# Optimization experiments

Hardware: AMD Instinct MI355X
Metric: run time of the kernel (lower is better)

The kernel has to match this reference:

```python
import jax, jax.numpy as jnp
import numpy as np

LATENT = 16
CTRL = 8
BLN = 128
MU = 0.1
EPS = 0.01
DT = 1.0
HID = 64


def _mlp(x, W1, b1, W2, b2, W3, b3):
    # two-hidden-layer tanh MLP (matches nn.Sequential(Linear,Tanh,Linear,Tanh,Linear))
    h = jnp.tanh(x @ W1.T + b1)
    h = jnp.tanh(h @ W2.T + b2)
    return h @ W3.T + b3


def setup_inputs() -> dict:
    key = jax.random.key(0)
    ks = jax.random.split(key, 16)
    B = 131072

    def w(k, shape):
        fan_in = shape[-1]
        return (jax.random.normal(k, shape, dtype=jnp.float32) / np.sqrt(fan_in)).astype(jnp.float32)

    inp = {
        "z": jax.random.normal(ks[0], (B, LATENT), dtype=jnp.float32),
        "u": jax.random.normal(ks[1], (B, CTRL), dtype=jnp.float32),
        # PLNet/BiLipNet Hamiltonian surrogate params: H(z)=0.5||mu*z + W_h2 tanh(W_h1 z + b_h1)||^2
        "Wh1": w(ks[2], (BLN, LATENT)),
        "bh1": jnp.zeros((BLN,), dtype=jnp.float32),
        "Wh2": w(ks[3], (LATENT, BLN)) * 0.5,
        # JR_net: latent -> 64 -> 64 -> 2*latent^2
        "W1_jr": w(ks[4], (HID, LATENT)),
        "b1_jr": jnp.zeros((HID,), dtype=jnp.float32),
        "W2_jr": w(ks[5], (HID, HID)),
        "b2_jr": jnp.zeros((HID,), dtype=jnp.float32),
        "W3_jr": w(ks[6], (2 * LATENT * LATENT, HID)) * 0.1,
        "b3_jr": jnp.zeros((2 * LATENT * LATENT,), dtype=jnp.float32),
        # Bnet: latent -> 64 -> 64 -> latent*control
        "W1_b": w(ks[7], (HID, LATENT)),
        "b1_b": jnp.zeros((HID,), dtype=jnp.float32),
        "W2_b": w(ks[8], (HID, HID)),
        "b2_b": jnp.zeros((HID,), dtype=jnp.float32),
        "W3_b": w(ks[9], (LATENT * CTRL, HID)) * 0.1,
        "b3_b": jnp.zeros((LATENT * CTRL,), dtype=jnp.float32),
    }
    return inp


def _compute_dz_and_output(z, u, Wh1, bh1, Wh2,
                           W1_jr, b1_jr, W2_jr, b2_jr, W3_jr, b3_jr,
                           W1_b, b1_b, W2_b, b2_b, W3_b, b3_b):
    B = z.shape[0]
    d = LATENT

    # H(z) = 0.5 ||f(z)||^2, f = mu*z + Wh2 tanh(Wh1 z + bh1)  (PLNet over BiLipNet surrogate)
    def H_sum(zz):
        f = MU * zz + jnp.tanh(zz @ Wh1.T + bh1) @ Wh2.T
        return 0.5 * jnp.sum(f * f)

    gH = jax.grad(H_sum)(z)                                  # [B, d]

    JR_out = _mlp(z, W1_jr, b1_jr, W2_jr, b2_jr, W3_jr, b3_jr)  # [B, 2d^2]
    Jm = JR_out[:, : d * d].reshape(B, d, d)
    Rf = JR_out[:, d * d:].reshape(B, d, d)
    J = Jm - jnp.swapaxes(Jm, 1, 2)                          # skew-symmetric
    R = jnp.einsum("bik,bjk->bij", Rf, Rf)                    # PSD

    Bmat = _mlp(z, W1_b, b1_b, W2_b, b2_b, W3_b, b3_b).reshape(B, d, CTRL)
    Bu = jnp.einsum("bdm,bm->bd", Bmat, u)

    dz = jnp.einsum("bij,bj->bi", J - R, gH) + Bu - EPS * gH
    y_pred = jnp.einsum("bdm,bd->bm", Bmat, gH)
    return dz, y_pred


def reference(z, u, Wh1, bh1, Wh2,
              W1_jr, b1_jr, W2_jr, b2_jr, W3_jr, b3_jr,
              W1_b, b1_b, W2_b, b2_b, W3_b, b3_b):
    args = (Wh1, bh1, Wh2, W1_jr, b1_jr, W2_jr, b2_jr, W3_jr, b3_jr,
            W1_b, b1_b, W2_b, b2_b, W3_b, b3_b)
    dz1, _ = _compute_dz_and_output(z, u, *args)
    z1 = z + DT * dz1
    dz2, y_pred = _compute_dz_and_output(z1, u, *args)
    z_next = z + 0.5 * DT * (dz1 + dz2)
    return (z_next, y_pred)
```

## Files before the change

### kernel.cpp

```cpp
#include <hip/hip_runtime.h>

#define THREADS 256
#define MU_C  0.1f
#define EPS_C 0.01f

typedef short bf16x8 __attribute__((ext_vector_type(8)));
typedef bf16x8 bf16x8_a __attribute__((may_alias));
typedef float f32x4 __attribute__((ext_vector_type(4)));
typedef f32x4 f32x4_a __attribute__((may_alias));
typedef float f32_a __attribute__((may_alias));
typedef unsigned uint2v __attribute__((ext_vector_type(2)));
typedef uint2v uint2_a __attribute__((may_alias));
typedef unsigned u32_a __attribute__((may_alias));
typedef unsigned short u16_a __attribute__((may_alias));

#define MFMA(a, b, c) __builtin_amdgcn_mfma_f32_16x16x32_bf16((a), (b), (c), 0, 0, 0)

#define T_WH1   0
#define T_WH2   8
#define T_WH2T  12
#define T_WH1T  20
#define T_W1JR  24
#define T_W2JR  28
#define T_JMN   36
#define T_JMT   68
#define T_RFN   100
#define T_RFT   132
#define T_W1B   164
#define T_W2B   168
#define T_BMN   176
#define T_BMT   192
#define T_JBN   208
#define T_JBT   209
#define T_RBN   210
#define T_RBT   211
#define T_BBN   212
#define NTILES  213

__device__ __forceinline__ float ftanh(float x) {
    float e = __builtin_amdgcn_exp2f(x * 2.88539008177792681472f);
    return 1.0f - 2.0f * __builtin_amdgcn_rcpf(e + 1.0f);
}
__device__ __forceinline__ short bfrn(float f) {
    unsigned u = __float_as_uint(f);
    return (short)((u + 0x8000u) >> 16);
}
__device__ __forceinline__ float bf2f(unsigned lo16) {
    return __uint_as_float(lo16 << 16);
}
__device__ __forceinline__ unsigned pk2(float lo, float hi) {
    return ((unsigned)(unsigned short)bfrn(hi) << 16) | (unsigned short)bfrn(lo);
}
__device__ __forceinline__ bf16x8 wsB(const short* __restrict__ ws, int tile, int lane) {
    return *reinterpret_cast<const bf16x8*>(ws + (size_t)((tile << 6) + lane) * 8);
}
__device__ __forceinline__ bf16x8 ldsA(const short* base, int strideS, int lane, int k0) {
    return *reinterpret_cast<const bf16x8_a*>(base + (lane & 15) * strideS + k0 + (lane >> 4) * 8);
}

__global__ __launch_bounds__(256)
void pack_weights(const float* __restrict__ Wh1, const float* __restrict__ bh1,
                  const float* __restrict__ Wh2,
                  const float* __restrict__ W1jr, const float* __restrict__ b1jr,
                  const float* __restrict__ W2jr, const float* __restrict__ W3jr,
                  const float* __restrict__ b3jr,
                  const float* __restrict__ W1b, const float* __restrict__ b1b,
                  const float* __restrict__ W2b, const float* __restrict__ W3b,
                  const float* __restrict__ b3b,
                  short* __restrict__ ws)
{
    const int id = blockIdx.x * 256 + threadIdx.x;
    if (id >= NTILES * 64) return;
    const int tile = id >> 6, lane = id & 63;
    const int j2 = lane & 15, g = lane >> 4;
    bf16x8 f;
#pragma unroll
    for (int jj = 0; jj < 8; ++jj) {
        const int k = g * 8 + jj;
        float x = 0.f;
        if (tile < T_WH2) {
            int n0 = (tile - T_WH1) * 16;
            if (g < 2) x = Wh1[(n0 + j2) * 16 + k];
            else if (k == 16) x = bh1[n0 + j2];
        } else if (tile < T_WH2T) {
            int kt = tile - T_WH2;
            x = Wh2[j2 * 128 + kt * 32 + k];
        } else if (tile < T_WH1T) {
            if (g < 2) x = Wh2[k * 128 + (tile - T_WH2T) * 16 + j2];
        } else if (tile < T_W1JR) {
            int kt = tile - T_WH1T;
            x = Wh1[(kt * 32 + k) * 16 + j2];
        } else if (tile < T_W2JR) {
            int n0 = (tile - T_W1JR) * 16;
            if (g < 2) x = W1jr[(n0 + j2) * 16 + k];
            else if (k == 16) x = b1jr[n0 + j2];
        } else if (tile < T_JMN) {
            int q = tile - T_W2JR; int nt = q >> 1, kt = q & 1;
            x = W2jr[(nt * 16 + j2) * 64 + kt * 32 + k];
        } else if (tile < T_JMT) {
            int q = tile - T_JMN; int n = q >> 1, kt = q & 1;
            x = W3jr[(n * 16 + j2) * 64 + kt * 32 + k];
        } else if (tile < T_RFN) {
            int q = tile - T_JMT; int t = q >> 1, kt = q & 1;
            x = W3jr[(j2 * 16 + t) * 64 + kt * 32 + k];
        } else if (tile < T_RFT) {
            int q = tile - T_RFN; int n = q >> 1, kt = q & 1;
            x = W3jr[(256 + n * 16 + j2) * 64 + kt * 32 + k];
        } else if (tile < T_W1B) {
            int q = tile - T_RFT; int t = q >> 1, kt = q & 1;
            x = W3jr[(256 + j2 * 16 + t) * 64 + kt * 32 + k];
        } else if (tile < T_W2B) {
            int n0 = (tile - T_W1B) * 16;
            if (g < 2) x = W1b[(n0 + j2) * 16 + k];
            else if (k == 16) x = b1b[n0 + j2];
        } else if (tile < T_BMN) {
            int q = tile - T_W2B; int nt = q >> 1, kt = q & 1;
            x = W2b[(nt * 16 + j2) * 64 + kt * 32 + k];
        } else if (tile < T_BMT) {
            int q = tile - T_BMN; int n = q >> 1, kt = q & 1;
            x = W3b[(n * 16 + j2) * 64 + kt * 32 + k];
        } else if (tile < T_JBN) {
            int q = tile - T_BMT; int m = q >> 1, kt = q & 1;
            x = W3b[(j2 * 8 + m) * 64 + kt * 32 + k];
        } else if (tile == T_JBN) {
            if (k < 16) x = b3jr[k * 16 + j2];
        } else if (tile == T_JBT) {
            if (k < 16) x = b3jr[j2 * 16 + k];
        } else if (tile == T_RBN) {
            if (k < 16) x = b3jr[256 + k * 16 + j2];
        } else if (tile == T_RBT) {
            if (k < 16) x = b3jr[256 + j2 * 16 + k];
        } else {
            if (k < 16 && j2 < 8) x = b3b[k * 8 + j2];
        }
        f[jj] = bfrn(x);
    }
    reinterpret_cast<bf16x8*>(ws)[id] = f;
}

struct __align__(16) WaveLds {
    short zt [16 * 40];
    short fvt[16 * 40];
    char  act[4608];
    float gHf[16 * 20];
    float uf [16 * 9];
};
struct __align__(16) BlockLds {
    WaveLds w[4];
    float bias[256];
};

__global__ __launch_bounds__(THREADS)
__attribute__((amdgpu_waves_per_eu(2, 4)))
void ph_mfma_kernel(const float* __restrict__ zg, const float* __restrict__ ug,
                    const float* __restrict__ b2jr, const float* __restrict__ b2b,
                    const float* __restrict__ b3b,
                    const short* __restrict__ ws,
                    float* __restrict__ out, int B)
{
    __shared__ BlockLds L;
    const int tid  = threadIdx.x;
    const int lane = tid & 63;
    const int wid  = tid >> 6;
    const int j2   = lane & 15;
    const int g    = lane >> 4;
    const int g4   = g * 4;
    const int rowbase = blockIdx.x * 64 + wid * 16;
    if (blockIdx.x * 64 >= B) return;

    WaveLds& Wv = L.w[wid];
    short* t1s = (short*)Wv.act;
    short* h1t = (short*)Wv.act;
    short* h2t = (short*)(Wv.act + 2304);
    short* rft = (short*)Wv.act;

    if (tid < 256) {
        float v;
        if      (tid < 64)  v = b2jr[tid];
        else if (tid < 128) v = b2b[tid - 64];
        else                v = b3b[tid - 128];
        L.bias[tid] = v;
    }
    if (lane < 16) {
        u32_a* p = (u32_a*)&Wv.zt[lane * 40 + 16];
        p[0] = 0x00003F80u;
#pragma unroll
        for (int i = 1; i < 8; ++i) p[i] = 0u;
        u32_a* q = (u32_a*)&Wv.fvt[lane * 40 + 16];
#pragma unroll
        for (int i = 0; i < 8; ++i) q[i] = 0u;
    }
    for (int i = lane; i < 128; i += 64) {
        int r = i >> 3, m = i & 7;
        Wv.uf[r * 9 + m] = ug[(size_t)(rowbase + r) * 8 + m];
    }
    float zReg[4];
    {
        float4 zv = *reinterpret_cast<const float4*>(zg + (size_t)(rowbase + j2) * 16 + g4);
        zReg[0] = zv.x; zReg[1] = zv.y; zReg[2] = zv.z; zReg[3] = zv.w;
        *(uint2_a*)&Wv.zt[j2 * 40 + g4] = (uint2v){pk2(zv.x, zv.y), pk2(zv.z, zv.w)};
    }
    __syncthreads();

#pragma unroll 1
    for (int pass = 0; pass < 2; ++pass) {
        bf16x8 bZ = ldsA(Wv.zt, 40, lane, 0);
        float dzAcc[4], fvReg[4];

#pragma unroll 4
        for (int nt = 0; nt < 8; ++nt) {
            f32x4 acc = {0.f, 0.f, 0.f, 0.f};
            acc = MFMA(wsB(ws, T_WH1 + nt, lane), bZ, acc);
            unsigned p0 = pk2(ftanh(acc[0]), ftanh(acc[1]));
            unsigned p1 = pk2(ftanh(acc[2]), ftanh(acc[3]));
            *(uint2_a*)&t1s[j2 * 136 + nt * 16 + g4] = (uint2v){p0, p1};
        }
        {
            f32x4 acc = {0.f, 0.f, 0.f, 0.f};
#pragma unroll 2
            for (int kt = 0; kt < 4; ++kt)
                acc = MFMA(wsB(ws, T_WH2 + kt, lane), ldsA(t1s, 136, lane, kt * 32), acc);
#pragma unroll
            for (int r = 0; r < 4; ++r) fvReg[r] = acc[r] + MU_C * zReg[r];
            *(uint2_a*)&Wv.fvt[j2 * 40 + g4] = (uint2v){pk2(fvReg[0], fvReg[1]), pk2(fvReg[2], fvReg[3])};
        }
        {
            bf16x8 bF = ldsA(Wv.fvt, 40, lane, 0);
#pragma unroll 4
            for (int nt = 0; nt < 8; ++nt) {
                f32x4 acc = {0.f, 0.f, 0.f, 0.f};
                acc = MFMA(wsB(ws, T_WH2T + nt, lane), bF, acc);
                uint2v tp = *(const uint2_a*)&t1s[j2 * 136 + nt * 16 + g4];
                float t0 = bf2f(tp[0] & 0xffffu), t1v = bf2f(tp[0] >> 16);
                float t2 = bf2f(tp[1] & 0xffffu), t3 = bf2f(tp[1] >> 16);
                unsigned p0 = pk2((1.f - t0 * t0) * acc[0], (1.f - t1v * t1v) * acc[1]);
                unsigned p1 = pk2((1.f - t2 * t2) * acc[2], (1.f - t3 * t3) * acc[3]);
                *(uint2_a*)&t1s[j2 * 136 + nt * 16 + g4] = (uint2v){p0, p1};
            }
        }
        {
            f32x4 acc = {0.f, 0.f, 0.f, 0.f};
#pragma unroll 2
            for (int kt = 0; kt < 4; ++kt)
                acc = MFMA(wsB(ws, T_WH1T + kt, lane), ldsA(t1s, 136, lane, kt * 32), acc);
            float gh0 = acc[0] + MU_C * fvReg[0], gh1 = acc[1] + MU_C * fvReg[1];
            float gh2 = acc[2] + MU_C * fvReg[2], gh3 = acc[3] + MU_C * fvReg[3];
            *(f32x4_a*)&Wv.gHf[j2 * 20 + g4] = (f32x4){gh0, gh1, gh2, gh3};
            *(uint2_a*)&Wv.fvt[j2 * 40 + g4] = (uint2v){pk2(gh0, gh1), pk2(gh2, gh3)};
            dzAcc[0] = -EPS_C * gh0; dzAcc[1] = -EPS_C * gh1;
            dzAcc[2] = -EPS_C * gh2; dzAcc[3] = -EPS_C * gh3;
        }
#pragma unroll 2
        for (int nt = 0; nt < 4; ++nt) {
            f32x4 acc = {0.f, 0.f, 0.f, 0.f};
            acc = MFMA(wsB(ws, T_W1JR + nt, lane), bZ, acc);
            *(uint2_a*)&h1t[j2 * 72 + nt * 16 + g4] =
                (uint2v){pk2(ftanh(acc[0]), ftanh(acc[1])), pk2(ftanh(acc[2]), ftanh(acc[3]))};
        }
        {
            bf16x8 b0 = ldsA(h1t, 72, lane, 0);
            bf16x8 b1 = ldsA(h1t, 72, lane, 32);
#pragma unroll 2
            for (int nt = 0; nt < 4; ++nt) {
                f32x4 acc = {0.f, 0.f, 0.f, 0.f};
                acc = MFMA(wsB(ws, T_W2JR + nt * 2 + 0, lane), b0, acc);
                acc = MFMA(wsB(ws, T_W2JR + nt * 2 + 1, lane), b1, acc);
                *(uint2_a*)&h2t[j2 * 72 + nt * 16 + g4] =
                    (uint2v){pk2(ftanh(acc[0] + L.bias[nt * 16 + g4 + 0]),
                                 ftanh(acc[1] + L.bias[nt * 16 + g4 + 1])),
                             pk2(ftanh(acc[2] + L.bias[nt * 16 + g4 + 2]),
                                 ftanh(acc[3] + L.bias[nt * 16 + g4 + 3]))};
            }
        }
        {
            bf16x8 bH0 = ldsA(h2t, 72, lane, 0);
            bf16x8 bH1 = ldsA(h2t, 72, lane, 32);
            bf16x8 bG  = ldsA(Wv.fvt, 40, lane, 0);
            {
                f32x4 bn = {0.f, 0.f, 0.f, 0.f};
                bn = MFMA(wsB(ws, T_JBN, lane), bG, bn);
                f32x4 bt = {0.f, 0.f, 0.f, 0.f};
                bt = MFMA(wsB(ws, T_JBT, lane), bG, bt);
#pragma unroll
                for (int r = 0; r < 4; ++r) dzAcc[r] += bt[r] - bn[r];
            }
#pragma unroll 4
            for (int n = 0; n < 16; ++n) {
                f32x4 acc = {0.f, 0.f, 0.f, 0.f};
                acc = MFMA(wsB(ws, T_JMN + 2 * n + 0, lane), bH0, acc);
                acc = MFMA(wsB(ws, T_JMN + 2 * n + 1, lane), bH1, acc);
                float gh = *(const f32_a*)&Wv.gHf[j2 * 20 + n];
#pragma unroll
                for (int r = 0; r < 4; ++r) dzAcc[r] -= acc[r] * gh;
            }
#pragma unroll 4
            for (int t = 0; t < 16; ++t) {
                f32x4 acc = {0.f, 0.f, 0.f, 0.f};
                acc = MFMA(wsB(ws, T_JMT + 2 * t + 0, lane), bH0, acc);
                acc = MFMA(wsB(ws, T_JMT + 2 * t + 1, lane), bH1, acc);
                float gh = *(const f32_a*)&Wv.gHf[j2 * 20 + t];
#pragma unroll
                for (int r = 0; r < 4; ++r) dzAcc[r] += acc[r] * gh;
            }
            {
                float rAcc[4] = {0.f, 0.f, 0.f, 0.f};
#pragma unroll 4
                for (int n = 0; n < 16; ++n) {
                    f32x4 acc = {0.f, 0.f, 0.f, 0.f};
                    acc = MFMA(wsB(ws, T_RFN + 2 * n + 0, lane), bH0, acc);
                    acc = MFMA(wsB(ws, T_RFN + 2 * n + 1, lane), bH1, acc);
                    float gh = *(const f32_a*)&Wv.gHf[j2 * 20 + n];
#pragma unroll
                    for (int r = 0; r < 4; ++r) rAcc[r] += acc[r] * gh;
                }
                f32x4 rb = {0.f, 0.f, 0.f, 0.f};
                rb = MFMA(wsB(ws, T_RBN, lane), bG, rb);
#pragma unroll
                for (int r = 0; r < 4; ++r) rAcc[r] += rb[r];
                *(uint2_a*)&rft[j2 * 40 + g4] = (uint2v){pk2(rAcc[0], rAcc[1]), pk2(rAcc[2], rAcc[3])};
                if (lane < 16) {
                    u32_a* p = (u32_a*)&rft[lane * 40 + 16];
#pragma unroll
                    for (int i = 0; i < 8; ++i) p[i] = 0u;
                }
            }
            {
                f32x4 rtb = {0.f, 0.f, 0.f, 0.f};
                rtb = MFMA(wsB(ws, T_RBT, lane), ldsA(rft, 40, lane, 0), rtb);
#pragma unroll
                for (int r = 0; r < 4; ++r) dzAcc[r] -= rtb[r];
            }
#pragma unroll 4
            for (int t = 0; t < 16; ++t) {
                f32x4 acc = {0.f, 0.f, 0.f, 0.f};
                acc = MFMA(wsB(ws, T_RFT + 2 * t + 0, lane), bH0, acc);
                acc = MFMA(wsB(ws, T_RFT + 2 * t + 1, lane), bH1, acc);
                float rv = bf2f(*(const u16_a*)&rft[j2 * 40 + t]);
#pragma unroll
                for (int r = 0; r < 4; ++r) dzAcc[r] -= acc[r] * rv;
            }
        }
#pragma unroll 2
        for (int nt = 0; nt < 4; ++nt) {
            f32x4 acc = {0.f, 0.f, 0.f, 0.f};
            acc = MFMA(wsB(ws, T_W1B + nt, lane), bZ, acc);
            *(uint2_a*)&h1t[j2 * 72 + nt * 16 + g4] =
                (uint2v){pk2(ftanh(acc[0]), ftanh(acc[1])), pk2(ftanh(acc[2]), ftanh(acc[3]))};
        }
        {
            bf16x8 b0 = ldsA(h1t, 72, lane, 0);
            bf16x8 b1 = ldsA(h1t, 72, lane, 32);
#pragma unroll 2
            for (int nt = 0; nt < 4; ++nt) {
                f32x4 acc = {0.f, 0.f, 0.f, 0.f};
                acc = MFMA(wsB(ws, T_W2B + nt * 2 + 0, lane), b0, acc);
                acc = MFMA(wsB(ws, T_W2B + nt * 2 + 1, lane), b1, acc);
                *(uint2_a*)&h2t[j2 * 72 + nt * 16 + g4] =
                    (uint2v){pk2(ftanh(acc[0] + L.bias[64 + nt * 16 + g4 + 0]),
                                 ftanh(acc[1] + L.bias[64 + nt * 16 + g4 + 1])),
                             pk2(ftanh(acc[2] + L.bias[64 + nt * 16 + g4 + 2]),
                                 ftanh(acc[3] + L.bias[64 + nt * 16 + g4 + 3]))};
            }
        }
        float yAcc[4] = {0.f, 0.f, 0.f, 0.f};
        f32x4 yb = {0.f, 0.f, 0.f, 0.f};
        {
            bf16x8 b0 = ldsA(h2t, 72, lane, 0);
            bf16x8 b1 = ldsA(h2t, 72, lane, 32);
            bf16x8 bG = ldsA(Wv.fvt, 40, lane, 0);
            yb = MFMA(wsB(ws, T_BBN, lane), bG, yb);
#pragma unroll 4
            for (int n = 0; n < 8; ++n) {
                f32x4 acc = {0.f, 0.f, 0.f, 0.f};
                acc = MFMA(wsB(ws, T_BMN + 2 * n + 0, lane), b0, acc);
                acc = MFMA(wsB(ws, T_BMN + 2 * n + 1, lane), b1, acc);
                float gh = *(const f32_a*)&Wv.gHf[j2 * 20 + 2 * n + (g >> 1)];
#pragma unroll
                for (int r = 0; r < 4; ++r) yAcc[r] += acc[r] * gh;
            }
#pragma unroll 4
            for (int m = 0; m < 8; ++m) {
                f32x4 acc = {0.f, 0.f, 0.f, 0.f};
                acc = MFMA(wsB(ws, T_BMT + 2 * m + 0, lane), b0, acc);
                acc = MFMA(wsB(ws, T_BMT + 2 * m + 1, lane), b1, acc);
                float um = *(const f32_a*)&Wv.uf[j2 * 9 + m];
#pragma unroll
                for (int r = 0; r < 4; ++r)
                    dzAcc[r] += (acc[r] + L.bias[128 + (g4 + r) * 8 + m]) * um;
            }
        }
        float* op = out + (size_t)(rowbase + j2) * 16 + g4;
        if (pass == 0) {
            float4 o;
            o.x = zReg[0] + 0.5f * dzAcc[0]; o.y = zReg[1] + 0.5f * dzAcc[1];
            o.z = zReg[2] + 0.5f * dzAcc[2]; o.w = zReg[3] + 0.5f * dzAcc[3];
            *reinterpret_cast<float4*>(op) = o;
#pragma unroll
            for (int r = 0; r < 4; ++r) zReg[r] += dzAcc[r];
            *(uint2_a*)&Wv.zt[j2 * 40 + g4] = (uint2v){pk2(zReg[0], zReg[1]), pk2(zReg[2], zReg[3])};
        } else {
            float4 o = *reinterpret_cast<const float4*>(op);
            o.x += 0.5f * dzAcc[0]; o.y += 0.5f * dzAcc[1];
            o.z += 0.5f * dzAcc[2]; o.w += 0.5f * dzAcc[3];
            *reinterpret_cast<float4*>(op) = o;
            float yv0 = yAcc[0] + __shfl_xor(yAcc[0], 32) + yb[0];
            float yv1 = yAcc[1] + __shfl_xor(yAcc[1], 32) + yb[1];
            float yv2 = yAcc[2] + __shfl_xor(yAcc[2], 32) + yb[2];
            float yv3 = yAcc[3] + __shfl_xor(yAcc[3], 32) + yb[3];
            if (g < 2) {
                float4 ys; ys.x = yv0; ys.y = yv1; ys.z = yv2; ys.w = yv3;
                *reinterpret_cast<float4*>(out + (size_t)B * 16 + (size_t)(rowbase + j2) * 8 + g4) = ys;
            }
        }
    }
}

extern "C" void kernel_launch(void* const* d_in, const int* in_sizes, int n_in,
                              void* d_out, int out_size, void* d_ws, size_t ws_size,
                              hipStream_t stream) {
    const float* zg   = (const float*)d_in[0];
    const float* ug   = (const float*)d_in[1];
    const float* Wh1  = (const float*)d_in[2];
    const float* bh1  = (const float*)d_in[3];
    const float* Wh2  = (const float*)d_in[4];
    const float* W1jr = (const float*)d_in[5];
    const float* b1jr = (const float*)d_in[6];
    const float* W2jr = (const float*)d_in[7];
    const float* b2jr = (const float*)d_in[8];
    const float* W3jr = (const float*)d_in[9];
    const float* b3jr = (const float*)d_in[10];
    const float* W1b  = (const float*)d_in[11];
    const float* b1b  = (const float*)d_in[12];
    const float* W2b  = (const float*)d_in[13];
    const float* b2b  = (const float*)d_in[14];
    const float* W3b  = (const float*)d_in[15];
    const float* b3b  = (const float*)d_in[16];

    short* ws = (short*)d_ws;
    const int B = in_sizes[0] / 16;

    hipLaunchKernelGGL(pack_weights, dim3((NTILES * 64 + 255) / 256), dim3(256), 0, stream,
                       Wh1, bh1, Wh2, W1jr, b1jr, W2jr, W3jr, b3jr,
                       W1b, b1b, W2b, W3b, b3b, ws);

    const int grid = (B + 63) / 64;
    hipLaunchKernelGGL(ph_mfma_kernel, dim3(grid), dim3(THREADS), 0, stream,
                       zg, ug, b2jr, b2b, b3b, ws, (float*)d_out, B);
}
```

Baseline: 115.3 us.

## Process two 16-row tiles per wave to reuse weight fragments across MFMAs

Each wave now handles 32 rows as two independent 16-row tiles. Every weight fragment loaded from global memory feeds two MFMAs instead of one, and the two independent accumulator chains add instruction-level parallelism. Per-wave LDS buffers are duplicated and the grid is halved. The cost is doubled LDS and higher register pressure per block, which may lower occupancy. The bias term of y is now folded into the accumulator before the cross-lane reduction.

```diff
diff --git a/kernel.cpp b/kernel.cpp
--- a/kernel.cpp
+++ b/kernel.cpp
@@ -14,7 +14,10 @@
 typedef unsigned u32_a __attribute__((may_alias));
 typedef unsigned short u16_a __attribute__((may_alias));
 
-#define MFMA(a, b, c) __builtin_amdgcn_mfma_f32_16x16x32_bf16((a), (b), (c), 0, 0, 0)
+__device__ __forceinline__ f32x4 MFMA(bf16x8 a, bf16x8 b, f32x4 c) {
+    return __builtin_amdgcn_mfma_f32_16x16x32_bf16(a, b, c, 0, 0, 0);
+}
+__device__ __forceinline__ f32x4 Z4() { f32x4 z = {0.f, 0.f, 0.f, 0.f}; return z; }
 
 #define T_WH1   0
 #define T_WH2   8
@@ -139,11 +142,11 @@
 }
 
 struct __align__(16) WaveLds {
-    short zt [16 * 40];
-    short fvt[16 * 40];
-    char  act[4608];
-    float gHf[16 * 20];
-    float uf [16 * 9];
+    short zt [2][16 * 40];
+    short fvt[2][16 * 40];
+    char  act[2][4608];
+    float gHf[2][16 * 20];
+    float uf [2][16 * 9];
 };
 struct __align__(16) BlockLds {
     WaveLds w[4];
@@ -165,14 +168,14 @@
     const int j2   = lane & 15;
     const int g    = lane >> 4;
     const int g4   = g * 4;
-    const int rowbase = blockIdx.x * 64 + wid * 16;
-    if (blockIdx.x * 64 >= B) return;
+    const int rowbase = blockIdx.x * 128 + wid * 32;
+    if (blockIdx.x * 128 >= B) return;
 
     WaveLds& Wv = L.w[wid];
-    short* t1s = (short*)Wv.act;
-    short* h1t = (short*)Wv.act;
-    short* h2t = (short*)(Wv.act + 2304);
-    short* rft = (short*)Wv.act;
+    short* t1p[2] = {(short*)Wv.act[0], (short*)Wv.act[1]};
+    short* h1p[2] = {(short*)Wv.act[0], (short*)Wv.act[1]};
+    short* h2p[2] = {(short*)(Wv.act[0] + 2304), (short*)(Wv.act[1] + 2304)};
+    short* rfp[2] = {(short*)Wv.act[0], (short*)Wv.act[1]};
 
     if (tid < 256) {
         float v;
@@ -182,234 +185,340 @@
         L.bias[tid] = v;
     }
     if (lane < 16) {
-        u32_a* p = (u32_a*)&Wv.zt[lane * 40 + 16];
-        p[0] = 0x00003F80u;
-#pragma unroll
-        for (int i = 1; i < 8; ++i) p[i] = 0u;
-        u32_a* q = (u32_a*)&Wv.fvt[lane * 40 + 16];
-#pragma unroll
-        for (int i = 0; i < 8; ++i) q[i] = 0u;
+#pragma unroll
+        for (int rt = 0; rt < 2; ++rt) {
+            u32_a* p = (u32_a*)&Wv.zt[rt][lane * 40 + 16];
+            p[0] = 0x00003F80u;
+#pragma unroll
+            for (int i = 1; i < 8; ++i) p[i] = 0u;
+            u32_a* q = (u32_a*)&Wv.fvt[rt][lane * 40 + 16];
+#pragma unroll
+            for (int i = 0; i < 8; ++i) q[i] = 0u;
+        }
     }
-    for (int i = lane; i < 128; i += 64) {
-        int r = i >> 3, m = i & 7;
-        Wv.uf[r * 9 + m] = ug[(size_t)(rowbase + r) * 8 + m];
+    for (int i = lane; i < 256; i += 64) {
+        int rt = i >> 7, r = (i >> 3) & 15, m = i & 7;
+        Wv.uf[rt][r * 9 + m] = ug[(size_t)(rowbase + rt * 16 + r) * 8 + m];
     }
-    float zReg[4];
-    {
-        float4 zv = *reinterpret_cast<const float4*>(zg + (size_t)(rowbase + j2) * 16 + g4);
-        zReg[0] = zv.x; zReg[1] = zv.y; zReg[2] = zv.z; zReg[3] = zv.w;
-        *(uint2_a*)&Wv.zt[j2 * 40 + g4] = (uint2v){pk2(zv.x, zv.y), pk2(zv.z, zv.w)};
+    float zReg[2][4];
+#pragma unroll
+    for (int rt = 0; rt < 2; ++rt) {
+        float4 zv = *reinterpret_cast<const float4*>(zg + (size_t)(rowbase + rt * 16 + j2) * 16 + g4);
+        zReg[rt][0] = zv.x; zReg[rt][1] = zv.y; zReg[rt][2] = zv.z; zReg[rt][3] = zv.w;
+        *(uint2_a*)&Wv.zt[rt][j2 * 40 + g4] = (uint2v){pk2(zv.x, zv.y), pk2(zv.z, zv.w)};
     }
     __syncthreads();
 
 #pragma unroll 1
     for (int pass = 0; pass < 2; ++pass) {
-        bf16x8 bZ = ldsA(Wv.zt, 40, lane, 0);
-        float dzAcc[4], fvReg[4];
-
-#pragma unroll 4
+        bf16x8 bZ0 = ldsA(Wv.zt[0], 40, lane, 0);
+        bf16x8 bZ1 = ldsA(Wv.zt[1], 40, lane, 0);
+        float dzAcc[2][4], fvReg[2][4];
+
+#pragma unroll 2
         for (int nt = 0; nt < 8; ++nt) {
-            f32x4 acc = {0.f, 0.f, 0.f, 0.f};
-            acc = MFMA(wsB(ws, T_WH1 + nt, lane), bZ, acc);
-            unsigned p0 = pk2(ftanh(acc[0]), ftanh(acc[1]));
-            unsigned p1 = pk2(ftanh(acc[2]), ftanh(acc[3]));
-            *(uint2_a*)&t1s[j2 * 136 + nt * 16 + g4] = (uint2v){p0, p1};
-        }
-        {
-            f32x4 acc = {0.f, 0.f, 0.f, 0.f};
-#pragma unroll 2
-            for (int kt = 0; kt < 4; ++kt)
-                acc = MFMA(wsB(ws, T_WH2 + kt, lane), ldsA(t1s, 136, lane, kt * 32), acc);
-#pragma unroll
-            for (int r = 0; r < 4; ++r) fvReg[r] = acc[r] + MU_C * zReg[r];
-            *(uint2_a*)&Wv.fvt[j2 * 40 + g4] = (uint2v){pk2(fvReg[0], fvReg[1]), pk2(fvReg[2], fvReg[3])};
-        }
-        {
-            bf16x8 bF = ldsA(Wv.fvt, 40, lane, 0);
-#pragma unroll 4
+            bf16x8 wt = wsB(ws, T_WH1 + nt, lane);
+            f32x4 a0 = MFMA(wt, bZ0, Z4());
+            f32x4 a1 = MFMA(wt, bZ1, Z4());
+            *(uint2_a*)&t1p[0][j2 * 136 + nt * 16 + g4] =
+                (uint2v){pk2(ftanh(a0[0]), ftanh(a0[1])), pk2(ftanh(a0[2]), ftanh(a0[3]))};
+            *(uint2_a*)&t1p[1][j2 * 136 + nt * 16 + g4] =
+                (uint2v){pk2(ftanh(a1[0]), ftanh(a1[1])), pk2(ftanh(a1[2]), ftanh(a1[3]))};
+        }
+        {
+            f32x4 a0 = Z4(), a1 = Z4();
+#pragma unroll 2
+            for (int kt = 0; kt < 4; ++kt) {
+                bf16x8 wt = wsB(ws, T_WH2 + kt, lane);
+                a0 = MFMA(wt, ldsA(t1p[0], 136, lane, kt * 32), a0);
+                a1 = MFMA(wt, ldsA(t1p[1], 136, lane, kt * 32), a1);
+            }
+#pragma unroll
+            for (int r = 0; r < 4; ++r) {
+                fvReg[0][r] = a0[r] + MU_C * zReg[0][r];
+                fvReg[1][r] = a1[r] + MU_C * zReg[1][r];
+            }
+            *(uint2_a*)&Wv.fvt[0][j2 * 40 + g4] =
+                (uint2v){pk2(fvReg[0][0], fvReg[0][1]), pk2(fvReg[0][2], fvReg[0][3])};
+            *(uint2_a*)&Wv.fvt[1][j2 * 40 + g4] =
+                (uint2v){pk2(fvReg[1][0], fvReg[1][1]), pk2(fvReg[1][2], fvReg[1][3])};
+        }
+        {
+            bf16x8 bF0 = ldsA(Wv.fvt[0], 40, lane, 0);
+            bf16x8 bF1 = ldsA(Wv.fvt[1], 40, lane, 0);
+#pragma unroll 2
             for (int nt = 0; nt < 8; ++nt) {
-                f32x4 acc = {0.f, 0.f, 0.f, 0.f};
-                acc = MFMA(wsB(ws, T_WH2T + nt, lane), bF, acc);
-                uint2v tp = *(const uint2_a*)&t1s[j2 * 136 + nt * 16 + g4];
-                float t0 = bf2f(tp[0] & 0xffffu), t1v = bf2f(tp[0] >> 16);
-                float t2 = bf2f(tp[1] & 0xffffu), t3 = bf2f(tp[1] >> 16);
-                unsigned p0 = pk2((1.f - t0 * t0) * acc[0], (1.f - t1v * t1v) * acc[1]);
-                unsigned p1 = pk2((1.f - t2 * t2) * acc[2], (1.f - t3 * t3) * acc[3]);
-                *(uint2_a*)&t1s[j2 * 136 + nt * 16 + g4] = (uint2v){p0, p1};
-            }
-        }
-        {
-            f32x4 acc = {0.f, 0.f, 0.f, 0.f};
-#pragma unroll 2
-            for (int kt = 0; kt < 4; ++kt)
-                acc = MFMA(wsB(ws, T_WH1T + kt, lane), ldsA(t1s, 136, lane, kt * 32), acc);
-            float gh0 = acc[0] + MU_C * fvReg[0], gh1 = acc[1] + MU_C * fvReg[1];
-            float gh2 = acc[2] + MU_C * fvReg[2], gh3 = acc[3] + MU_C * fvReg[3];
-            *(f32x4_a*)&Wv.gHf[j2 * 20 + g4] = (f32x4){gh0, gh1, gh2, gh3};
-            *(uint2_a*)&Wv.fvt[j2 * 40 + g4] = (uint2v){pk2(gh0, gh1), pk2(gh2, gh3)};
-            dzAcc[0] = -EPS_C * gh0; dzAcc[1] = -EPS_C * gh1;
-            dzAcc[2] = -EPS_C * gh2; dzAcc[3] = -EPS_C * gh3;
+                bf16x8 wt = wsB(ws, T_WH2T + nt, lane);
+                f32x4 a0 = MFMA(wt, bF0, Z4());
+                f32x4 a1 = MFMA(wt, bF1, Z4());
+#pragma unroll
+                for (int rt = 0; rt < 2; ++rt) {
+                    f32x4 aa = rt ? a1 : a0;
+                    uint2v tp = *(const uint2_a*)&t1p[rt][j2 * 136 + nt * 16 + g4];
+                    float t0 = bf2f(tp[0] & 0xffffu), t1v = bf2f(tp[0] >> 16);
+                    float t2 = bf2f(tp[1] & 0xffffu), t3 = bf2f(tp[1] >> 16);
+                    *(uint2_a*)&t1p[rt][j2 * 136 + nt * 16 + g4] =
+                        (uint2v){pk2((1.f - t0 * t0) * aa[0], (1.f - t1v * t1v) * aa[1]),
+                                 pk2((1.f - t2 * t2) * aa[2], (1.f - t3 * t3) * aa[3])};
+                }
+            }
+        }
+        {
+            f32x4 a0 = Z4(), a1 = Z4();
+#pragma unroll 2
+            for (int kt = 0; kt < 4; ++kt) {
+                bf16x8 wt = wsB(ws, T_WH1T + kt, lane);
+                a0 = MFMA(wt, ldsA(t1p[0], 136, lane, kt * 32), a0);
+                a1 = MFMA(wt, ldsA(t1p[1], 136, lane, kt * 32), a1);
+            }
+#pragma unroll
+            for (int rt = 0; rt < 2; ++rt) {
+                f32x4 aa = rt ? a1 : a0;
+                float gh0 = aa[0] + MU_C * fvReg[rt][0], gh1 = aa[1] + MU_C * fvReg[rt][1];
+                float gh2 = aa[2] + MU_C * fvReg[rt][2], gh3 = aa[3] + MU_C * fvReg[rt][3];
+                *(f32x4_a*)&Wv.gHf[rt][j2 * 20 + g4] = (f32x4){gh0, gh1, gh2, gh3};
+                *(uint2_a*)&Wv.fvt[rt][j2 * 40 + g4] = (uint2v){pk2(gh0, gh1), pk2(gh2, gh3)};
+                dzAcc[rt][0] = -EPS_C * gh0; dzAcc[rt][1] = -EPS_C * gh1;
+                dzAcc[rt][2] = -EPS_C * gh2; dzAcc[rt][3] = -EPS_C * gh3;
+            }
         }
 #pragma unroll 2
         for (int nt = 0; nt < 4; ++nt) {
-            f32x4 acc = {0.f, 0.f, 0.f, 0.f};
-            acc = MFMA(wsB(ws, T_W1JR + nt, lane), bZ, acc);
-            *(uint2_a*)&h1t[j2 * 72 + nt * 16 + g4] =
-                (uint2v){pk2(ftanh(acc[0]), ftanh(acc[1])), pk2(ftanh(acc[2]), ftanh(acc[3]))};
-        }
-        {
-            bf16x8 b0 = ldsA(h1t, 72, lane, 0);
-            bf16x8 b1 = ldsA(h1t, 72, lane, 32);
+            bf16x8 wt = wsB(ws, T_W1JR + nt, lane);
+            f32x4 a0 = MFMA(wt, bZ0, Z4());
+            f32x4 a1 = MFMA(wt, bZ1, Z4());
+            *(uint2_a*)&h1p[0][j2 * 72 + nt * 16 + g4] =
+                (uint2v){pk2(ftanh(a0[0]), ftanh(a0[1])), pk2(ftanh(a0[2]), ftanh(a0[3]))};
+            *(uint2_a*)&h1p[1][j2 * 72 + nt * 16 + g4] =
+                (uint2v){pk2(ftanh(a1[0]), ftanh(a1[1])), pk2(ftanh(a1[2]), ftanh(a1[3]))};
+        }
+        {
+            bf16x8 c00 = ldsA(h1p[0], 72, lane, 0), c01 = ldsA(h1p[0], 72, lane, 32);
+            bf16x8 c10 = ldsA(h1p[1], 72, lane, 0), c11 = ldsA(h1p[1], 72, lane, 32);
 #pragma unroll 2
             for (int nt = 0; nt < 4; ++nt) {
-                f32x4 acc = {0.f, 0.f, 0.f, 0.f};
-                acc = MFMA(wsB(ws, T_W2JR + nt * 2 + 0, lane), b0, acc);
-                acc = MFMA(wsB(ws, T_W2JR + nt * 2 + 1, lane), b1, acc);
-                *(uint2_a*)&h2t[j2 * 72 + nt * 16 + g4] =
-                    (uint2v){pk2(ftanh(acc[0] + L.bias[nt * 16 + g4 + 0]),
-                                 ftanh(acc[1] + L.bias[nt * 16 + g4 + 1])),
-                             pk2(ftanh(acc[2] + L.bias[nt * 16 + g4 + 2]),
-                                 ftanh(acc[3] + L.bias[nt * 16 + g4 + 3]))};
-            }
-        }
-        {
-            bf16x8 bH0 = ldsA(h2t, 72, lane, 0);
-            bf16x8 bH1 = ldsA(h2t, 72, lane, 32);
-            bf16x8 bG  = ldsA(Wv.fvt, 40, lane, 0);
+                bf16x8 w0 = wsB(ws, T_W2JR + nt * 2 + 0, lane);
+                bf16x8 w1 = wsB(ws, T_W2JR + nt * 2 + 1, lane);
+                f32x4 a0 = MFMA(w1, c01, MFMA(w0, c00, Z4()));
+                f32x4 a1 = MFMA(w1, c11, MFMA(w0, c10, Z4()));
+#pragma unroll
+                for (int rt = 0; rt < 2; ++rt) {
+                    f32x4 aa = rt ? a1 : a0;
+                    *(uint2_a*)&h2p[rt][j2 * 72 + nt * 16 + g4] =
+                        (uint2v){pk2(ftanh(aa[0] + L.bias[nt * 16 + g4 + 0]),
+                                     ftanh(aa[1] + L.bias[nt * 16 + g4 + 1])),
+                                 pk2(ftanh(aa[2] + L.bias[nt * 16 + g4 + 2]),
+                                     ftanh(aa[3] + L.bias[nt * 16 + g4 + 3]))};
+                }
+            }
+        }
+        {
+            bf16x8 h00 = ldsA(h2p[0], 72, lane, 0), h01 = ldsA(h2p[0], 72, lane, 32);
+            bf16x8 h10 = ldsA(h2p[1], 72, lane, 0), h11 = ldsA(h2p[1], 72, lane, 32);
+            bf16x8 bG0 = ldsA(Wv.fvt[0], 40, lane, 0);
+            bf16x8 bG1 = ldsA(Wv.fvt[1], 40, lane, 0);
             {
-                f32x4 bn = {0.f, 0.f, 0.f, 0.f};
-                bn = MFMA(wsB(ws, T_JBN, lane), bG, bn);
-                f32x4 bt = {0.f, 0.f, 0.f, 0.f};
-                bt = MFMA(wsB(ws, T_JBT, lane), bG, bt);
-#pragma unroll
-                for (int r = 0; r < 4; ++r) dzAcc[r] += bt[r] - bn[r];
-            }
-#pragma unroll 4
+                bf16x8 wn = wsB(ws, T_JBN, lane);
+                bf16x8 wtt = wsB(ws, T_JBT, lane);
+                f32x4 bn0 = MFMA(wn, bG0, Z4());
+                f32x4 bn1 = MFMA(wn, bG1, Z4());
+                f32x4 bt0 = MFMA(wtt, bG0, Z4());
+                f32x4 bt1 = MFMA(wtt, bG1, Z4());
+#pragma unroll
+                for (int r = 0; r < 4; ++r) {
+                    dzAcc[0][r] += bt0[r] - bn0[r];
+                    dzAcc[1][r] += bt1[r] - bn1[r];
+                }
+            }
+#pragma unroll 2
             for (int n = 0; n < 16; ++n) {
-                f32x4 acc = {0.f, 0.f, 0.f, 0.f};
-                acc = MFMA(wsB(ws, T_JMN + 2 * n + 0, lane), bH0, acc);
-                acc = MFMA(wsB(ws, T_JMN + 2 * n + 1, lane), bH1, acc);
-                float gh = *(const f32_a*)&Wv.gHf[j2 * 20 + n];
-#pragma unroll
-                for (int r = 0; r < 4; ++r) dzAcc[r] -= acc[r] * gh;
-            }
-#pragma unroll 4
+                bf16x8 w0 = wsB(ws, T_JMN + 2 * n + 0, lane);
+                bf16x8 w1 = wsB(ws, T_JMN + 2 * n + 1, lane);
+                f32x4 a0 = MFMA(w1, h01, MFMA(w0, h00, Z4()));
+                f32x4 a1 = MFMA(w1, h11, MFMA(w0, h10, Z4()));
+                float gA = *(const f32_a*)&Wv.gHf[0][j2 * 20 + n];
+                float gB = *(const f32_a*)&Wv.gHf[1][j2 * 20 + n];
+#pragma unroll
+                for (int r = 0; r < 4; ++r) {
+                    dzAcc[0][r] -= a0[r] * gA;
+                    dzAcc[1][r] -= a1[r] * gB;
+                }
+            }
+#pragma unroll 2
             for (int t = 0; t < 16; ++t) {
-                f32x4 acc = {0.f, 0.f, 0.f, 0.f};
-                acc = MFMA(wsB(ws, T_JMT + 2 * t + 0, lane), bH0, acc);
-                acc = MFMA(wsB(ws, T_JMT + 2 * t + 1, lane), bH1, acc);
-                float gh = *(const f32_a*)&Wv.gHf[j2 * 20 + t];
-#pragma unroll
-                for (int r = 0; r < 4; ++r) dzAcc[r] += acc[r] * gh;
+                bf16x8 w0 = wsB(ws, T_JMT + 2 * t + 0, lane);
+                bf16x8 w1 = wsB(ws, T_JMT + 2 * t + 1, lane);
+                f32x4 a0 = MFMA(w1, h01, MFMA(w0, h00, Z4()));
+                f32x4 a1 = MFMA(w1, h11, MFMA(w0, h10, Z4()));
+                float gA = *(const f32_a*)&Wv.gHf[0][j2 * 20 + t];
+                float gB = *(const f32_a*)&Wv.gHf[1][j2 * 20 + t];
+#pragma unroll
+                for (int r = 0; r < 4; ++r) {
+                    dzAcc[0][r] += a0[r] * gA;
+                    dzAcc[1][r] += a1[r] * gB;
+                }
             }
             {
-                float rAcc[4] = {0.f, 0.f, 0.f, 0.f};
-#pragma unroll 4
+                float rA[2][4] = {{0.f, 0.f, 0.f, 0.f}, {0.f, 0.f, 0.f, 0.f}};
+#pragma unroll 2
                 for (int n = 0; n < 16; ++n) {
-                    f32x4 acc = {0.f, 0.f, 0.f, 0.f};
-                    acc = MFMA(wsB(ws, T_RFN + 2 * n + 0, lane), bH0, acc);
-                    acc = MFMA(wsB(ws, T_RFN + 2 * n + 1, lane), bH1, acc);
-                    float gh = *(const f32_a*)&Wv.gHf[j2 * 20 + n];
-#pragma unroll
-                    for (int r = 0; r < 4; ++r) rAcc[r] += acc[r] * gh;
-                }
-                f32x4 rb = {0.f, 0.f, 0.f, 0.f};
-                rb = MFMA(wsB(ws, T_RBN, lane), bG, rb);
-#pragma unroll
-                for (int r = 0; r < 4; ++r) rAcc[r] += rb[r];
-                *(uint2_a*)&rft[j2 * 40 + g4] = (uint2v){pk2(rAcc[0], rAcc[1]), pk2(rAcc[2], rAcc[3])};
+                    bf16x8 w0 = wsB(ws, T_RFN + 2 * n + 0, lane);
+                    bf16x8 w1 = wsB(ws, T_RFN + 2 * n + 1, lane);
+                    f32x4 a0 = MFMA(w1, h01, MFMA(w0, h00, Z4()));
+                    f32x4 a1 = MFMA(w1, h11, MFMA(w0, h10, Z4()));
+                    float gA = *(const f32_a*)&Wv.gHf[0][j2 * 20 + n];
+                    float gB = *(const f32_a*)&Wv.gHf[1][j2 * 20 + n];
+#pragma unroll
+                    for (int r = 0; r < 4; ++r) {
+                        rA[0][r] += a0[r] * gA;
+                        rA[1][r] += a1[r] * gB;
+                    }
+                }
+                bf16x8 wrb = wsB(ws, T_RBN, lane);
+                f32x4 rb0 = MFMA(wrb, bG0, Z4());
+                f32x4 rb1 = MFMA(wrb, bG1, Z4());
+                *(uint2_a*)&rfp[0][j2 * 40 + g4] =
+                    (uint2v){pk2(rA[0][0] + rb0[0], rA[0][1] + rb0[1]),
+                             pk2(rA[0][2] + rb0[2], rA[0][3] + rb0[3])};
+                *(uint2_a*)&rfp[1][j2 * 40 + g4] =
+                    (uint2v){pk2(rA[1][0] + rb1[0], rA[1][1] + rb1[1]),
+                             pk2(rA[1][2] + rb1[2], rA[1][3] + rb1[3])};
                 if (lane < 16) {
-                    u32_a* p = (u32_a*)&rft[lane * 40 + 16];
-#pragma unroll
-                    for (int i = 0; i < 8; ++i) p[i] = 0u;
+#pragma unroll
+                    for (int rt = 0; rt < 2; ++rt) {
+                        u32_a* p = (u32_a*)&rfp[rt][lane * 40 + 16];
+#pragma unroll
+                        for (int i = 0; i < 8; ++i) p[i] = 0u;
+                    }
                 }
             }
             {
-                f32x4 rtb = {0.f, 0.f, 0.f, 0.f};
-                rtb = MFMA(wsB(ws, T_RBT, lane), ldsA(rft, 40, lane, 0), rtb);
-#pragma unroll
-                for (int r = 0; r < 4; ++r) dzAcc[r] -= rtb[r];
-            }
-#pragma unroll 4
+                bf16x8 wrt = wsB(ws, T_RBT, lane);
+                f32x4 rtb0 = MFMA(wrt, ldsA(rfp[0], 40, lane, 0), Z4());
+                f32x4 rtb1 = MFMA(wrt, ldsA(rfp[1], 40, lane, 0), Z4());
+#pragma unroll
+                for (int r = 0; r < 4; ++r) {
+                    dzAcc[0][r] -= rtb0[r];
+                    dzAcc[1][r] -= rtb1[r];
+                }
+            }
+#pragma unroll 2
             for (int t = 0; t < 16; ++t) {
-                f32x4 acc = {0.f, 0.f, 0.f, 0.f};
-                acc = MFMA(wsB(ws, T_RFT + 2 * t + 0, lane), bH0, acc);
-                acc = MFMA(wsB(ws, T_RFT + 2 * t + 1, lane), bH1, acc);
-                float rv = bf2f(*(const u16_a*)&rft[j2 * 40 + t]);
-#pragma unroll
-                for (int r = 0; r < 4; ++r) dzAcc[r] -= acc[r] * rv;
+                bf16x8 w0 = wsB(ws, T_RFT + 2 * t + 0, lane);
+                bf16x8 w1 = wsB(ws, T_RFT + 2 * t + 1, lane);
+                f32x4 a0 = MFMA(w1, h01, MFMA(w0, h00, Z4()));
+                f32x4 a1 = MFMA(w1, h11, MFMA(w0, h10, Z4()));
+                float rvA = bf2f(*(const u16_a*)&rfp[0][j2 * 40 + t]);
+                float rvB = bf2f(*(const u16_a*)&rfp[1][j2 * 40 + t]);
+#pragma unroll
+                for (int r = 0; r < 4; ++r) {
+                    dzAcc[0][r] -= a0[r] * rvA;
+                    dzAcc[1][r] -= a1[r] * rvB;
+                }
             }
         }
 #pragma unroll 2
         for (int nt = 0; nt < 4; ++nt) {
-            f32x4 acc = {0.f, 0.f, 0.f, 0.f};
-            acc = MFMA(wsB(ws, T_W1B + nt, lane), bZ, acc);
-            *(uint2_a*)&h1t[j2 * 72 + nt * 16 + g4] =
-                (uint2v){pk2(ftanh(acc[0]), ftanh(acc[1])), pk2(ftanh(acc[2]), ftanh(acc[3]))};
-        }
-        {
-            bf16x8 b0 = ldsA(h1t, 72, lane, 0);
-            bf16x8 b1 = ldsA(h1t, 72, lane, 32);
+            bf16x8 wt = wsB(ws, T_W1B + nt, lane);
+            f32x4 a0 = MFMA(wt, bZ0, Z4());
+            f32x4 a1 = MFMA(wt, bZ1, Z4());
+            *(uint2_a*)&h1p[0][j2 * 72 + nt * 16 + g4] =
+                (uint2v){pk2(ftanh(a0[0]), ftanh(a0[1])), pk2(ftanh(a0[2]), ftanh(a0[3]))};
+            *(uint2_a*)&h1p[1][j2 * 72 + nt * 16 + g4] =
+                (uint2v){pk2(ftanh(a1[0]), ftanh(a1[1])), pk2(ftanh(a1[2]), ftanh(a1[3]))};
+        }
+        {
+            bf16x8 c00 = ldsA(h1p[0], 72, lane, 0), c01 = ldsA(h1p[0], 72, lane, 32);
+            bf16x8 c10 = ldsA(h1p[1], 72, lane, 0), c11 = ldsA(h1p[1], 72, lane, 32);
 #pragma unroll 2
             for (int nt = 0; nt < 4; ++nt) {
-                f32x4 acc = {0.f, 0.f, 0.f, 0.f};
-                acc = MFMA(wsB(ws, T_W2B + nt * 2 + 0, lane), b0, acc);
-                acc = MFMA(wsB(ws, T_W2B + nt * 2 + 1, lane), b1, acc);
-                *(uint2_a*)&h2t[j2 * 72 + nt * 16 + g4] =
-                    (uint2v){pk2(ftanh(acc[0] + L.bias[64 + nt * 16 + g4 + 0]),
-                                 ftanh(acc[1] + L.bias[64 + nt * 16 + g4 + 1])),
-                             pk2(ftanh(acc[2] + L.bias[64 + nt * 16 + g4 + 2]),
-                                 ftanh(acc[3] + L.bias[64 + nt * 16 + g4 + 3]))};
-            }
-        }
-        float yAcc[4] = {0.f, 0.f, 0.f, 0.f};
-        f32x4 yb = {0.f, 0.f, 0.f, 0.f};
-        {
-            bf16x8 b0 = ldsA(h2t, 72, lane, 0);
-            bf16x8 b1 = ldsA(h2t, 72, lane, 32);
-            bf16x8 bG = ldsA(Wv.fvt, 40, lane, 0);
-            yb = MFMA(wsB(ws, T_BBN, lane), bG, yb);
-#pragma unroll 4
+                bf16x8 w0 = wsB(ws, T_W2B + nt * 2 + 0, lane);
+                bf16x8 w1 = wsB(ws, T_W2B + nt * 2 + 1, lane);
+                f32x4 a0 = MFMA(w1, c01, MFMA(w0, c00, Z4()));
+                f32x4 a1 = MFMA(w1, c11, MFMA(w0, c10, Z4()));
+#pragma unroll
+                for (int rt = 0; rt < 2; ++rt) {
+                    f32x4 aa = rt ? a1 : a0;
+                    *(uint2_a*)&h2p[rt][j2 * 72 + nt * 16 + g4] =
+                        (uint2v){pk2(ftanh(aa[0] + L.bias[64 + nt * 16 + g4 + 0]),
+                                     ftanh(aa[1] + L.bias[64 + nt * 16 + g4 + 1])),
+                                 pk2(ftanh(aa[2] + L.bias[64 + nt * 16 + g4 + 2]),
+                                     ftanh(aa[3] + L.bias[64 + nt * 16 + g4 + 3]))};
+                }
+            }
+        }
+        float yAcc[2][4];
+        {
+            bf16x8 h00 = ldsA(h2p[0], 72, lane, 0), h01 = ldsA(h2p[0], 72, lane, 32);
+            bf16x8 h10 = ldsA(h2p[1], 72, lane, 0), h11 = ldsA(h2p[1], 72, lane, 32);
+            bf16x8 bG0 = ldsA(Wv.fvt[0], 40, lane, 0);
+            bf16x8 bG1 = ldsA(Wv.fvt[1], 40, lane, 0);
+            bf16x8 wbb = wsB(ws, T_BBN, lane);
+            f32x4 yb0 = MFMA(wbb, bG0, Z4());
+            f32x4 yb1 = MFMA(wbb, bG1, Z4());
+#pragma unroll
+            for (int r = 0; r < 4; ++r) {
+                yAcc[0][r] = yb0[r];
+                yAcc[1][r] = yb1[r];
+            }
+#pragma unroll 2
             for (int n = 0; n < 8; ++n) {
-                f32x4 acc = {0.f, 0.f, 0.f, 0.f};
-                acc = MFMA(wsB(ws, T_BMN + 2 * n + 0, lane), b0, acc);
-                acc = MFMA(wsB(ws, T_BMN + 2 * n + 1, lane), b1, acc);
-                float gh = *(const f32_a*)&Wv.gHf[j2 * 20 + 2 * n + (g >> 1)];
-#pragma unroll
-                for (int r = 0; r < 4; ++r) yAcc[r] += acc[r] * gh;
-            }
-#pragma unroll 4
+                bf16x8 w0 = wsB(ws, T_BMN + 2 * n + 0, lane);
+                bf16x8 w1 = wsB(ws, T_BMN + 2 * n + 1, lane);
+                f32x4 a0 = MFMA(w1, h01, MFMA(w0, h00, Z4()));
+                f32x4 a1 = MFMA(w1, h11, MFMA(w0, h10, Z4()));
+                float gA = *(const f32_a*)&Wv.gHf[0][j2 * 20 + 2 * n + (g >> 1)];
+                float gB = *(const f32_a*)&Wv.gHf[1][j2 * 20 + 2 * n + (g >> 1)];
+#pragma unroll
+                for (int r = 0; r < 4; ++r) {
+                    yAcc[0][r] += a0[r] * gA;
+                    yAcc[1][r] += a1[r] * gB;
+                }
+            }
+#pragma unroll 2
             for (int m = 0; m < 8; ++m) {
-                f32x4 acc = {0.f, 0.f, 0.f, 0.f};
-                acc = MFMA(wsB(ws, T_BMT + 2 * m + 0, lane), b0, acc);
-                acc = MFMA(wsB(ws, T_BMT + 2 * m + 1, lane), b1, acc);
-                float um = *(const f32_a*)&Wv.uf[j2 * 9 + m];
-#pragma unroll
-                for (int r = 0; r < 4; ++r)
-                    dzAcc[r] += (acc[r] + L.bias[128 + (g4 + r) * 8 + m]) * um;
-            }
-        }
-        float* op = out + (size_t)(rowbase + j2) * 16 + g4;
-        if (pass == 0) {
-            float4 o;
-            o.x = zReg[0] + 0.5f * dzAcc[0]; o.y = zReg[1] + 0.5f * dzAcc[1];
-            o.z = zReg[2] + 0.5f * dzAcc[2]; o.w = zReg[3] + 0.5f * dzAcc[3];
-            *reinterpret_cast<float4*>(op) = o;
-#pragma unroll
-            for (int r = 0; r < 4; ++r) zReg[r] += dzAcc[r];
-            *(uint2_a*)&Wv.zt[j2 * 40 + g4] = (uint2v){pk2(zReg[0], zReg[1]), pk2(zReg[2], zReg[3])};
-        } else {
-            float4 o = *reinterpret_cast<const float4*>(op);
-            o.x += 0.5f * dzAcc[0]; o.y += 0.5f * dzAcc[1];
-            o.z += 0.5f * dzAcc[2]; o.w += 0.5f * dzAcc[3];
-            *reinterpret_cast<float4*>(op) = o;
-            float yv0 = yAcc[0] + __shfl_xor(yAcc[0], 32) + yb[0];
-            float yv1 = yAcc[1] + __shfl_xor(yAcc[1], 32) + yb[1];
-            float yv2 = yAcc[2] + __shfl_xor(yAcc[2], 32) + yb[2];
-            float yv3 = yAcc[3] + __shfl_xor(yAcc[3], 32) + yb[3];
-            if (g < 2) {
-                float4 ys; ys.x = yv0; ys.y = yv1; ys.z = yv2; ys.w = yv3;
-                *reinterpret_cast<float4*>(out + (size_t)B * 16 + (size_t)(rowbase + j2) * 8 + g4) = ys;
+                bf16x8 w0 = wsB(ws, T_BMT + 2 * m + 0, lane);
+                bf16x8 w1 = wsB(ws, T_BMT + 2 * m + 1, lane);
+                f32x4 a0 = MFMA(w1, h01, MFMA(w0, h00, Z4()));
+                f32x4 a1 = MFMA(w1, h11, MFMA(w0, h10, Z4()));
+                float uA = *(const f32_a*)&Wv.uf[0][j2 * 9 + m];
+                float uB = *(const f32_a*)&Wv.uf[1][j2 * 9 + m];
+#pragma unroll
+                for (int r = 0; r < 4; ++r) {
+                    float bb = L.bias[128 + (g4 + r) * 8 + m];
+                    dzAcc[0][r] += (a0[r] + bb) * uA;
+                    dzAcc[1][r] += (a1[r] + bb) * uB;
+                }
+            }
+        }
+#pragma unroll
+        for (int rt = 0; rt < 2; ++rt) {
+            float* op = out + (size_t)(rowbase + rt * 16 + j2) * 16 + g4;
+            if (pass == 0) {
+                float4 o;
+                o.x = zReg[rt][0] + 0.5f * dzAcc[rt][0];
+                o.y = zReg[rt][1] + 0.5f * dzAcc[rt][1];
+                o.z = zReg[rt][2] + 0.5f * dzAcc[rt][2];
+                o.w = zReg[rt][3] + 0.5f * dzAcc[rt][3];
+                *reinterpret_cast<float4*>(op) = o;
+#pragma unroll
+                for (int r = 0; r < 4; ++r) zReg[rt][r] += dzAcc[rt][r];
+                *(uint2_a*)&Wv.zt[rt][j2 * 40 + g4] =
+                    (uint2v){pk2(zReg[rt][0], zReg[rt][1]), pk2(zReg[rt][2], zReg[rt][3])};
+            } else {
+                float4 o = *reinterpret_cast<const float4*>(op);
+                o.x += 0.5f * dzAcc[rt][0]; o.y += 0.5f * dzAcc[rt][1];
+                o.z += 0.5f * dzAcc[rt][2]; o.w += 0.5f * dzAcc[rt][3];
+                *reinterpret_cast<float4*>(op) = o;
+                float yv0 = yAcc[rt][0] + __shfl_xor(yAcc[rt][0], 32);
+                float yv1 = yAcc[rt][1] + __shfl_xor(yAcc[rt][1], 32);
+                float yv2 = yAcc[rt][2] + __shfl_xor(yAcc[rt][2], 32);
+                float yv3 = yAcc[rt][3] + __shfl_xor(yAcc[rt][3], 32);
+                if (g < 2) {
+                    float4 ys; ys.x = yv0; ys.y = yv1; ys.z = yv2; ys.w = yv3;
+                    *reinterpret_cast<float4*>(out + (size_t)B * 16 +
+                        (size_t)(rowbase + rt * 16 + j2) * 8 + g4) = ys;
+                }
             }
         }
     }
@@ -443,7 +552,7 @@
                        Wh1, bh1, Wh2, W1jr, b1jr, W2jr, W3jr, b3jr,
                        W1b, b1b, W2b, W3b, b3b, ws);
 
-    const int grid = (B + 63) / 64;
+    const int grid = (B + 127) / 128;
     hipLaunchKernelGGL(ph_mfma_kernel, dim3(grid), dim3(THREADS), 0, stream,
                        zg, ug, b2jr, b2b, b3b, ws, (float*)d_out, B);
 }
```

Result: faster. 104.4 us, median of 2 (-9.4%).
